# Kernel optimization log

Hardware: AMD Instinct MI355X
Metric: run time of the kernel (lower is better)

Reference implementation:

```python
import jax, jax.numpy as jnp
import numpy as np

HEADS = 16

def setup_inputs() -> dict:
    key = jax.random.key(0)
    ks = jax.random.split(key, 7)
    B, S, E = 2, 2048, 1024
    return {
        "query": jax.random.normal(ks[0], (B, S, E), dtype=jnp.float32),
        "key": jax.random.normal(ks[1], (B, S, E), dtype=jnp.float32),
        "value": jax.random.normal(ks[2], (B, S, E), dtype=jnp.float32),
        "Wqkv": jax.random.normal(ks[3], (E, 3 * E), dtype=jnp.float32) * (E ** -0.5),
        "bqkv": jax.random.normal(ks[4], (3 * E,), dtype=jnp.float32) * 0.02,
        "Wproj": jax.random.normal(ks[5], (E, E), dtype=jnp.float32) * (E ** -0.5),
        "bproj": jax.random.normal(ks[6], (E,), dtype=jnp.float32) * 0.02,
    }

def reference(query, key, value, Wqkv, bqkv, Wproj, bproj):
    # key/value args are unused in the original forward (overwritten by QKV split)
    B, S, E = query.shape
    H = HEADS
    hd = E // H
    qkv = query @ Wqkv + bqkv                     # [B, S, 3E]
    qkv = qkv.reshape(B, S, H, 3 * hd).transpose(0, 2, 1, 3)  # [B, H, S, 3hd]
    q = qkv[..., :hd]
    k = qkv[..., hd:2 * hd]
    v = qkv[..., 2 * hd:]
    qk = jnp.einsum("bhqd,bhkd->bhqk", q, k)
    # faithful quirk: original divides by head_dim**-0.5, i.e. multiplies by sqrt(hd)
    scaled = qk / (hd ** -0.5)
    attn = jax.nn.softmax(scaled, axis=-1)        # dropout p=0 -> identity
    out = jnp.einsum("bhqk,bhkd->bhqd", attn, v)  # [B, H, S, hd]
    out = out.transpose(0, 2, 1, 3).reshape(B, S, E)
    return out @ Wproj + bproj
```

## Files before the change

### kernel.cpp

```cpp
#include <hip/hip_runtime.h>
#include <hip/hip_bf16.h>
#include <stdint.h>

typedef __attribute__((ext_vector_type(8))) _Float16 f16x8;
typedef __attribute__((ext_vector_type(4))) _Float16 f16x4;
typedef __attribute__((ext_vector_type(4))) float f32x4;

static constexpr int BATCH = 2;
static constexpr int SEQ = 2048;
static constexpr int EMB = 1024;
static constexpr int NH = 16;
static constexpr int HD_ = 64;

#define AS1 __attribute__((address_space(1)))
#define AS3 __attribute__((address_space(3)))

__device__ __forceinline__ void gload_lds16(const void* g, void* l) {
  __builtin_amdgcn_global_load_lds((const AS1 uint32_t*)g, (AS3 uint32_t*)l, 16, 0, 0);
}

__device__ __forceinline__ f32x4 mfma16(f16x8 a, f16x8 b, f32x4 c) {
  return __builtin_amdgcn_mfma_f32_16x16x32_f16(a, b, c, 0, 0, 0);
}

__device__ __forceinline__ f16x8 swzread(const _Float16* base, int row, int blk) {
  return *(const f16x8*)((const char*)base + row * 128 +
                         ((blk * 16) ^ ((row & 7) << 4)));
}

__global__ __launch_bounds__(256) void k_prep(const float* __restrict__ q,
                                              _Float16* __restrict__ qo,
                                              const float* __restrict__ wqkv,
                                              _Float16* __restrict__ wqkvo,
                                              const float* __restrict__ wproj,
                                              _Float16* __restrict__ wprojo) {
  __shared__ float tile[32][33];
  const int blk = blockIdx.x;
  const int t = threadIdx.x;
  if (blk < 4096) {
    const int idx = blk * 256 + t;
    float4 v = reinterpret_cast<const float4*>(q)[idx];
    const float* f = reinterpret_cast<const float*>(&v);
    _Float16 h[4];
#pragma unroll
    for (int i = 0; i < 4; ++i) h[i] = (_Float16)f[i];
    reinterpret_cast<uint2*>(qo)[idx] = *reinterpret_cast<uint2*>(h);
    return;
  }
  const float* in;
  _Float16* out;
  int R, C, bx, by;
  bool perm;
  if (blk < 4096 + 3072) {
    const int lo = blk - 4096;
    bx = lo % 96;
    by = lo / 96;
    in = wqkv; out = wqkvo; R = 1024; C = 3072; perm = true;
  } else {
    const int lo = blk - 7168;
    bx = lo & 31;
    by = lo >> 5;
    in = wproj; out = wprojo; R = 1024; C = 1024; perm = false;
  }
  const int tr = t >> 5, tc = t & 31;
  const int r0 = by * 32, c0 = bx * 32;
#pragma unroll
  for (int rr = 0; rr < 32; rr += 8)
    tile[tr + rr][tc] = in[(size_t)(r0 + tr + rr) * C + c0 + tc];
  __syncthreads();
#pragma unroll
  for (int rr = 0; rr < 32; rr += 8) {
    const int c = c0 + tr + rr;
    int d = c;
    if (perm) {
      const int h = c / 192, r = c - h * 192;
      d = (r < 64) ? h * 64 + r
                   : (r < 128 ? 1024 + h * 64 + (r - 64) : 2048 + h * 64 + (r - 128));
    }
    out[(size_t)d * R + r0 + tc] = (_Float16)tile[tc][tr + rr];
  }
}

__global__ __launch_bounds__(512, 1) void k_gemm_qkv(const _Float16* __restrict__ A,
                                                     const _Float16* __restrict__ Bt,
                                                     const float* __restrict__ bias,
                                                     _Float16* __restrict__ oq,
                                                     _Float16* __restrict__ ok,
                                                     _Float16* __restrict__ ov) {
  constexpr int K = EMB;
  __shared__ _Float16 As[2][2][128 * 64];
  __shared__ _Float16 Bs[2][2][128 * 64];
  const int t = threadIdx.x;
  const int l = t & 63, w = t >> 6;
  const int lr = l & 15, lg = l >> 4;
  const int wm = w >> 2, wn = w & 3;
  const int id = blockIdx.x;
  const int xcd = id & 7, wg = id >> 3;
  const int m0 = (xcd * 2 + wg / 12) * 256;
  const int n0 = (wg % 12) * 256;

  const int sr0 = t >> 3, scb = t & 7;
  auto stageA = [&](int buf, int half, int kt) {
    const _Float16* g = A + (size_t)(m0 + half * 128) * K + kt * 64;
    _Float16* d = &As[buf][half][0];
    gload_lds16(g + (size_t)sr0 * K + (scb ^ (sr0 & 7)) * 8, d + sr0 * 64 + scb * 8);
    const int r1 = sr0 + 64;
    gload_lds16(g + (size_t)r1 * K + (scb ^ (r1 & 7)) * 8, d + r1 * 64 + scb * 8);
  };
  auto stageB = [&](int buf, int half, int kt) {
    const _Float16* g = Bt + (size_t)(n0 + half * 128) * K + kt * 64;
    _Float16* d = &Bs[buf][half][0];
    gload_lds16(g + (size_t)sr0 * K + (scb ^ (sr0 & 7)) * 8, d + sr0 * 64 + scb * 8);
    const int r1 = sr0 + 64;
    gload_lds16(g + (size_t)r1 * K + (scb ^ (r1 & 7)) * 8, d + r1 * 64 + scb * 8);
  };

  f32x4 acc[8][4];
#pragma unroll
  for (int m = 0; m < 8; ++m)
#pragma unroll
    for (int n = 0; n < 4; ++n) acc[m][n] = f32x4{0.f, 0.f, 0.f, 0.f};

  stageA(0, 0, 0);
  stageA(0, 1, 0);
  stageB(0, 0, 0);
  stageB(0, 1, 0);

  const int bhh = wn >> 1, brow0 = (wn & 1) * 64;
  f16x8 bf[4][2];

  for (int pair = 0; pair < 8; ++pair) {
#pragma unroll
    for (int ph = 0; ph < 8; ++ph) {
      const int buf = ph >> 2, q = ph & 3;
      bool issued = true;
      if (ph < 4) {
        const int kt = 2 * pair + 1;
        if (q == 0) stageA(1, 0, kt);
        else if (q == 1) stageA(1, 1, kt);
        else if (q == 2) stageB(1, 0, kt);
        else stageB(1, 1, kt);
      } else if (pair + 1 < 8) {
        const int kt = 2 * pair + 2;
        if (q == 0) stageA(0, 0, kt);
        else if (q == 1) stageA(0, 1, kt);
        else if (q == 2) stageB(0, 0, kt);
        else stageB(0, 1, kt);
      } else {
        issued = false;
      }
      if (q == 0) {
        if (issued)
          asm volatile("s_waitcnt vmcnt(2)" ::: "memory");
        else
          asm volatile("s_waitcnt vmcnt(0)" ::: "memory");
        __builtin_amdgcn_s_barrier();
#pragma unroll
        for (int nf = 0; nf < 4; ++nf)
#pragma unroll
          for (int ks = 0; ks < 2; ++ks)
            bf[nf][ks] = swzread(&Bs[buf][bhh][0], brow0 + nf * 16 + lr, ks * 4 + lg);
      }
      f16x8 af[2][2];
#pragma unroll
      for (int dm = 0; dm < 2; ++dm)
#pragma unroll
        for (int ks = 0; ks < 2; ++ks)
          af[dm][ks] = swzread(&As[buf][wm][0], (q * 2 + dm) * 16 + lr, ks * 4 + lg);
      __builtin_amdgcn_s_setprio(1);
#pragma unroll
      for (int dm = 0; dm < 2; ++dm)
#pragma unroll
        for (int nf = 0; nf < 4; ++nf)
#pragma unroll
          for (int ks = 0; ks < 2; ++ks)
            acc[q * 2 + dm][nf] =
                mfma16(af[dm][ks], bf[nf][ks], acc[q * 2 + dm][nf]);
      __builtin_amdgcn_s_setprio(0);
      __builtin_amdgcn_s_barrier();
    }
  }

  const int sec = n0 >> 10;
#pragma unroll
  for (int mf = 0; mf < 8; ++mf) {
#pragma unroll
    for (int nf = 0; nf < 4; ++nf) {
      const int col = n0 + wn * 64 + nf * 16 + lr;
      const int cc = col & 1023;
      const int h = cc >> 6, r = cc & 63;
      const float bv = bias[h * 192 + sec * 64 + r];
      const int row0 = m0 + wm * 128 + mf * 16 + lg * 4;
      const int b = row0 >> 11, s0 = row0 & (SEQ - 1);
      if (sec == 2) {
        f16x4 vv;
#pragma unroll
        for (int i = 0; i < 4; ++i) vv[i] = (_Float16)(acc[mf][nf][i] + bv);
        *(f16x4*)&ov[(((size_t)b * NH + h) * HD_ + r) * SEQ + s0] = vv;
      } else {
#pragma unroll
        for (int i = 0; i < 4; ++i) {
          const float v = acc[mf][nf][i] + bv;
          const size_t dst = (((size_t)b * NH + h) * SEQ + s0 + i) * HD_ + r;
          if (sec == 0)
            oq[dst] = (_Float16)(v * 11.5415603f);
          else
            ok[dst] = (_Float16)v;
        }
      }
    }
  }
}

__global__ __launch_bounds__(256) void k_gemm_proj(const _Float16* __restrict__ A,
                                                   const _Float16* __restrict__ Bt,
                                                   const float* __restrict__ bias,
                                                   float* __restrict__ of) {
  constexpr int K = EMB, N = EMB;
  __shared__ _Float16 As[2][128 * 32];
  __shared__ _Float16 Bs[2][128 * 32];
  const int t = threadIdx.x;
  const int l = t & 63, w = t >> 6;
  const int lr = l & 15, lg = l >> 4;
  const int wr = w >> 1, wc = w & 1;
  const int id = blockIdx.x;
  const int xcd = id & 7, wg = id >> 3;
  const int m0 = (xcd * 4 + wg / 8) * 128;
  const int n0 = (wg & 7) * 128;

  auto stage = [&](int buf, int k0) {
#pragma unroll
    for (int j = 0; j < 2; ++j) {
      const int c = t + 256 * j;
      const int row = c >> 2, cb = c & 3;
      gload_lds16(A + (size_t)(m0 + row) * K + k0 + cb * 8, &As[buf][c * 8]);
      gload_lds16(Bt + (size_t)(n0 + row) * K + k0 + cb * 8, &Bs[buf][c * 8]);
    }
  };

  f32x4 acc[4][4];
#pragma unroll
  for (int m = 0; m < 4; ++m)
#pragma unroll
    for (int n = 0; n < 4; ++n) acc[m][n] = f32x4{0.f, 0.f, 0.f, 0.f};

  stage(0, 0);
  const int NT = K / 32;
  int cur = 0;
  for (int kt = 0; kt < NT; ++kt) {
    __syncthreads();
    if (kt + 1 < NT) stage(cur ^ 1, (kt + 1) * 32);
    f16x8 af[4], bf[4];
#pragma unroll
    for (int m = 0; m < 4; ++m)
      af[m] = *(const f16x8*)&As[cur][(wr * 64 + m * 16 + lr) * 32 + lg * 8];
#pragma unroll
    for (int n = 0; n < 4; ++n)
      bf[n] = *(const f16x8*)&Bs[cur][(wc * 64 + n * 16 + lr) * 32 + lg * 8];
#pragma unroll
    for (int m = 0; m < 4; ++m)
#pragma unroll
      for (int n = 0; n < 4; ++n) acc[m][n] = mfma16(af[m], bf[n], acc[m][n]);
    cur ^= 1;
  }

#pragma unroll
  for (int m = 0; m < 4; ++m)
#pragma unroll
    for (int n = 0; n < 4; ++n)
#pragma unroll
      for (int i = 0; i < 4; ++i) {
        const int row = m0 + wr * 64 + m * 16 + lg * 4 + i;
        const int col = n0 + wc * 64 + n * 16 + lr;
        of[(size_t)row * N + col] = acc[m][n][i] + bias[col];
      }
}

__global__ __launch_bounds__(512) void k_attn(const _Float16* __restrict__ qs,
                                              const _Float16* __restrict__ ks,
                                              const _Float16* __restrict__ vt,
                                              _Float16* __restrict__ ao) {
  __shared__ _Float16 Kt[3][64][64];
  __shared__ _Float16 Vt[3][64][64];
  __shared__ _Float16 Pl[8][16][64];
  const int t = threadIdx.x;
  const int l = t & 63, w = t >> 6;
  const int lr = l & 15, lg = l >> 4;
  const int id = blockIdx.x;
  const int xc = id & 7, m_ = id >> 3;
  const int bh = xc + 8 * (m_ >> 4);
  const int qb = (m_ & 15) * 128 + w * 16;

  const size_t qoff = ((size_t)bh * SEQ + qb + lr) * HD_;
  const f16x8 qf0 = *(const f16x8*)(qs + qoff + lg * 8);
  const f16x8 qf1 = *(const f16x8*)(qs + qoff + 32 + lg * 8);

  const _Float16* kbase = ks + (size_t)bh * SEQ * HD_;
  const _Float16* vbase = vt + (size_t)bh * HD_ * SEQ;

  const int srow = t >> 3, scb = t & 7;
  auto stage = [&](const int buf, const int kv0) {
    gload_lds16(kbase + (size_t)(kv0 + srow) * HD_ + (scb ^ (srow & 7)) * 8,
                &Kt[buf][srow][scb * 8]);
    gload_lds16(vbase + (size_t)srow * SEQ + kv0 + (scb ^ (srow & 7)) * 8,
                &Vt[buf][srow][scb * 8]);
  };

  stage(0, 0);
  stage(1, 64);

  float mr = -1e30f, lsum = 0.f;
  f32x4 oacc[4];
#pragma unroll
  for (int n = 0; n < 4; ++n) oacc[n] = f32x4{0.f, 0.f, 0.f, 0.f};

  const int NT = SEQ / 64;
  int cur = 0;
  for (int it = 0; it < NT; ++it) {
    if (it == NT - 1)
      asm volatile("s_waitcnt vmcnt(0)" ::: "memory");
    else
      asm volatile("s_waitcnt vmcnt(2)" ::: "memory");
    __builtin_amdgcn_s_barrier();
    if (it + 2 < NT) {
      int nb = cur + 2;
      if (nb >= 3) nb -= 3;
      stage(nb, (it + 2) * 64);
    }

    f32x4 sa[4];
    __builtin_amdgcn_s_setprio(1);
#pragma unroll
    for (int t4 = 0; t4 < 4; ++t4) {
      const int r = t4 * 16 + lr;
      const f16x8 kf0 = swzread(&Kt[cur][0][0], r, lg);
      const f16x8 kf1 = swzread(&Kt[cur][0][0], r, lg + 4);
      f32x4 s = mfma16(kf0, qf0, f32x4{0.f, 0.f, 0.f, 0.f});
      sa[t4] = mfma16(kf1, qf1, s);
    }
    __builtin_amdgcn_s_setprio(0);

    float t01 = fmaxf(fmaxf(sa[0][0], sa[0][1]), fmaxf(sa[0][2], sa[0][3]));
    float t23 = fmaxf(fmaxf(sa[1][0], sa[1][1]), fmaxf(sa[1][2], sa[1][3]));
    float t45 = fmaxf(fmaxf(sa[2][0], sa[2][1]), fmaxf(sa[2][2], sa[2][3]));
    float t67 = fmaxf(fmaxf(sa[3][0], sa[3][1]), fmaxf(sa[3][2], sa[3][3]));
    float tm = fmaxf(fmaxf(t01, t23), fmaxf(t45, t67));
    tm = fmaxf(tm, __shfl_xor(tm, 16));
    tm = fmaxf(tm, __shfl_xor(tm, 32));

    if (__all(tm < mr - 24.0f)) {
      cur = (cur + 1 == 3) ? 0 : cur + 1;
      continue;
    }

    if (__any(tm > mr + 8.0f)) {
      const float nm = fmaxf(mr, tm);
      const float corr = exp2f(mr - nm);
      mr = nm;
      lsum *= corr;
      float cb4[4];
#pragma unroll
      for (int i = 0; i < 4; ++i)
        cb4[i] = __shfl(corr, (l & 48) + ((l >> 4) << 2) + i);
#pragma unroll
      for (int n = 0; n < 4; ++n)
#pragma unroll
        for (int i = 0; i < 4; ++i) oacc[n][i] *= cb4[i];
    }

    float ts = 0.f;
    char* plbase = (char*)&Pl[w][0][0];
#pragma unroll
    for (int t4 = 0; t4 < 4; ++t4) {
      f16x4 pp;
#pragma unroll
      for (int i = 0; i < 4; ++i) {
        const float p = exp2f(sa[t4][i] - mr);
        ts += p;
        pp[i] = (_Float16)p;
      }
      *(f16x4*)(plbase + lr * 128 + ((t4 * 32 + lg * 8) ^ ((lr & 7) << 4))) = pp;
    }
    ts += __shfl_xor(ts, 16);
    ts += __shfl_xor(ts, 32);
    lsum += ts;

    const f16x8 aP0 = swzread(&Pl[w][0][0], lr, lg);
    const f16x8 aP1 = swzread(&Pl[w][0][0], lr, lg + 4);
    __builtin_amdgcn_s_setprio(1);
#pragma unroll
    for (int n = 0; n < 4; ++n) {
      const int d = n * 16 + lr;
      const f16x8 bv0 = swzread(&Vt[cur][0][0], d, lg);
      const f16x8 bv1 = swzread(&Vt[cur][0][0], d, lg + 4);
      oacc[n] = mfma16(aP0, bv0, oacc[n]);
      oacc[n] = mfma16(aP1, bv1, oacc[n]);
    }
    __builtin_amdgcn_s_setprio(0);

    cur = (cur + 1 == 3) ? 0 : cur + 1;
  }

  float ls4[4];
#pragma unroll
  for (int i = 0; i < 4; ++i)
    ls4[i] = __shfl(lsum, (l & 48) + ((l >> 4) << 2) + i);
  const int b = bh >> 4, h = bh & 15;
#pragma unroll
  for (int n = 0; n < 4; ++n)
#pragma unroll
    for (int i = 0; i < 4; ++i) {
      const int row = qb + ((l >> 4) << 2) + i;
      ao[((size_t)b * SEQ + row) * EMB + h * HD_ + n * 16 + lr] =
          (_Float16)(oacc[n][i] / ls4[i]);
    }
}

extern "C" void kernel_launch(void* const* d_in, const int* in_sizes, int n_in,
                              void* d_out, int out_size, void* d_ws, size_t ws_size,
                              hipStream_t stream) {
  const float* query = (const float*)d_in[0];
  const float* Wqkv = (const float*)d_in[3];
  const float* bqkv = (const float*)d_in[4];
  const float* Wproj = (const float*)d_in[5];
  const float* bproj = (const float*)d_in[6];
  float* out = (float*)d_out;

  char* ws = (char*)d_ws;
  const size_t MB = 1024 * 1024;
  _Float16* q_f16   = (_Float16*)(ws + 0);
  _Float16* Wqkv_t  = (_Float16*)(ws + 16 * MB);
  _Float16* q_s     = (_Float16*)(ws + 24 * MB);
  _Float16* k_s     = (_Float16*)(ws + 32 * MB);
  _Float16* v_t     = (_Float16*)(ws + 40 * MB);
  _Float16* Wproj_t = (_Float16*)(ws + 48 * MB);
  _Float16* a_o     = (_Float16*)(ws + 51 * MB);

  const int M = BATCH * SEQ;
  k_prep<<<dim3(8192), 256, 0, stream>>>(query, q_f16, Wqkv, Wqkv_t, Wproj, Wproj_t);
  k_gemm_qkv<<<dim3(192), 512, 0, stream>>>(q_f16, Wqkv_t, bqkv, q_s, k_s, v_t);
  k_attn<<<dim3(512), 512, 0, stream>>>(q_s, k_s, v_t, a_o);
  k_gemm_proj<<<dim3(256), 256, 0, stream>>>(a_o, Wproj_t, bproj, out);
}
```

Measured before the change: 145.1 us.

## Switch attention KV staging to double-buffered 128-key tiles with one barrier

```diff
diff --git a/kernel.cpp b/kernel.cpp
--- a/kernel.cpp
+++ b/kernel.cpp
@@ -280,8 +280,8 @@
                                               const _Float16* __restrict__ ks,
                                               const _Float16* __restrict__ vt,
                                               _Float16* __restrict__ ao) {
-  __shared__ _Float16 Kt[3][64][64];
-  __shared__ _Float16 Vt[3][64][64];
+  __shared__ _Float16 Kt[2][128][64];
+  __shared__ _Float16 Vt[2][2][64][64];
   __shared__ _Float16 Pl[8][16][64];
   const int t = threadIdx.x;
   const int l = t & 63, w = t >> 6;
@@ -302,103 +302,97 @@
   auto stage = [&](const int buf, const int kv0) {
     gload_lds16(kbase + (size_t)(kv0 + srow) * HD_ + (scb ^ (srow & 7)) * 8,
                 &Kt[buf][srow][scb * 8]);
+    const int r1 = srow + 64;
+    gload_lds16(kbase + (size_t)(kv0 + r1) * HD_ + (scb ^ (srow & 7)) * 8,
+                &Kt[buf][r1][scb * 8]);
     gload_lds16(vbase + (size_t)srow * SEQ + kv0 + (scb ^ (srow & 7)) * 8,
-                &Vt[buf][srow][scb * 8]);
+                &Vt[buf][0][srow][scb * 8]);
+    gload_lds16(vbase + (size_t)srow * SEQ + kv0 + 64 + (scb ^ (srow & 7)) * 8,
+                &Vt[buf][1][srow][scb * 8]);
   };
 
   stage(0, 0);
-  stage(1, 64);
 
   float mr = -1e30f, lsum = 0.f;
   f32x4 oacc[4];
 #pragma unroll
   for (int n = 0; n < 4; ++n) oacc[n] = f32x4{0.f, 0.f, 0.f, 0.f};
 
-  const int NT = SEQ / 64;
-  int cur = 0;
+  char* plbase = (char*)&Pl[w][0][0];
+  const int NT = SEQ / 128;
   for (int it = 0; it < NT; ++it) {
-    if (it == NT - 1)
-      asm volatile("s_waitcnt vmcnt(0)" ::: "memory");
-    else
-      asm volatile("s_waitcnt vmcnt(2)" ::: "memory");
-    __builtin_amdgcn_s_barrier();
-    if (it + 2 < NT) {
-      int nb = cur + 2;
-      if (nb >= 3) nb -= 3;
-      stage(nb, (it + 2) * 64);
-    }
-
-    f32x4 sa[4];
-    __builtin_amdgcn_s_setprio(1);
-#pragma unroll
-    for (int t4 = 0; t4 < 4; ++t4) {
-      const int r = t4 * 16 + lr;
-      const f16x8 kf0 = swzread(&Kt[cur][0][0], r, lg);
-      const f16x8 kf1 = swzread(&Kt[cur][0][0], r, lg + 4);
-      f32x4 s = mfma16(kf0, qf0, f32x4{0.f, 0.f, 0.f, 0.f});
-      sa[t4] = mfma16(kf1, qf1, s);
-    }
-    __builtin_amdgcn_s_setprio(0);
-
-    float t01 = fmaxf(fmaxf(sa[0][0], sa[0][1]), fmaxf(sa[0][2], sa[0][3]));
-    float t23 = fmaxf(fmaxf(sa[1][0], sa[1][1]), fmaxf(sa[1][2], sa[1][3]));
-    float t45 = fmaxf(fmaxf(sa[2][0], sa[2][1]), fmaxf(sa[2][2], sa[2][3]));
-    float t67 = fmaxf(fmaxf(sa[3][0], sa[3][1]), fmaxf(sa[3][2], sa[3][3]));
-    float tm = fmaxf(fmaxf(t01, t23), fmaxf(t45, t67));
-    tm = fmaxf(tm, __shfl_xor(tm, 16));
-    tm = fmaxf(tm, __shfl_xor(tm, 32));
-
-    if (__all(tm < mr - 24.0f)) {
-      cur = (cur + 1 == 3) ? 0 : cur + 1;
-      continue;
-    }
-
-    if (__any(tm > mr + 8.0f)) {
-      const float nm = fmaxf(mr, tm);
-      const float corr = exp2f(mr - nm);
-      mr = nm;
-      lsum *= corr;
-      float cb4[4];
-#pragma unroll
-      for (int i = 0; i < 4; ++i)
-        cb4[i] = __shfl(corr, (l & 48) + ((l >> 4) << 2) + i);
-#pragma unroll
-      for (int n = 0; n < 4; ++n)
-#pragma unroll
-        for (int i = 0; i < 4; ++i) oacc[n][i] *= cb4[i];
-    }
-
-    float ts = 0.f;
-    char* plbase = (char*)&Pl[w][0][0];
-#pragma unroll
-    for (int t4 = 0; t4 < 4; ++t4) {
-      f16x4 pp;
-#pragma unroll
-      for (int i = 0; i < 4; ++i) {
-        const float p = exp2f(sa[t4][i] - mr);
-        ts += p;
-        pp[i] = (_Float16)p;
-      }
-      *(f16x4*)(plbase + lr * 128 + ((t4 * 32 + lg * 8) ^ ((lr & 7) << 4))) = pp;
-    }
-    ts += __shfl_xor(ts, 16);
-    ts += __shfl_xor(ts, 32);
-    lsum += ts;
-
-    const f16x8 aP0 = swzread(&Pl[w][0][0], lr, lg);
-    const f16x8 aP1 = swzread(&Pl[w][0][0], lr, lg + 4);
-    __builtin_amdgcn_s_setprio(1);
-#pragma unroll
-    for (int n = 0; n < 4; ++n) {
-      const int d = n * 16 + lr;
-      const f16x8 bv0 = swzread(&Vt[cur][0][0], d, lg);
-      const f16x8 bv1 = swzread(&Vt[cur][0][0], d, lg + 4);
-      oacc[n] = mfma16(aP0, bv0, oacc[n]);
-      oacc[n] = mfma16(aP1, bv1, oacc[n]);
-    }
-    __builtin_amdgcn_s_setprio(0);
-
-    cur = (cur + 1 == 3) ? 0 : cur + 1;
+    const int cur = it & 1;
+    __syncthreads();
+    if (it + 1 < NT) stage(cur ^ 1, (it + 1) * 128);
+
+#pragma unroll
+    for (int sub = 0; sub < 2; ++sub) {
+      f32x4 sa[4];
+      __builtin_amdgcn_s_setprio(1);
+#pragma unroll
+      for (int t4 = 0; t4 < 4; ++t4) {
+        const int r = sub * 64 + t4 * 16 + lr;
+        const f16x8 kf0 = swzread(&Kt[cur][0][0], r, lg);
+        const f16x8 kf1 = swzread(&Kt[cur][0][0], r, lg + 4);
+        f32x4 s = mfma16(kf0, qf0, f32x4{0.f, 0.f, 0.f, 0.f});
+        sa[t4] = mfma16(kf1, qf1, s);
+      }
+      __builtin_amdgcn_s_setprio(0);
+
+      float t01 = fmaxf(fmaxf(sa[0][0], sa[0][1]), fmaxf(sa[0][2], sa[0][3]));
+      float t23 = fmaxf(fmaxf(sa[1][0], sa[1][1]), fmaxf(sa[1][2], sa[1][3]));
+      float t45 = fmaxf(fmaxf(sa[2][0], sa[2][1]), fmaxf(sa[2][2], sa[2][3]));
+      float t67 = fmaxf(fmaxf(sa[3][0], sa[3][1]), fmaxf(sa[3][2], sa[3][3]));
+      float tm = fmaxf(fmaxf(t01, t23), fmaxf(t45, t67));
+      tm = fmaxf(tm, __shfl_xor(tm, 16));
+      tm = fmaxf(tm, __shfl_xor(tm, 32));
+
+      if (__all(tm < mr - 24.0f)) continue;
+
+      if (__any(tm > mr + 8.0f)) {
+        const float nm = fmaxf(mr, tm);
+        const float corr = exp2f(mr - nm);
+        mr = nm;
+        lsum *= corr;
+        float cb4[4];
+#pragma unroll
+        for (int i = 0; i < 4; ++i)
+          cb4[i] = __shfl(corr, (l & 48) + ((l >> 4) << 2) + i);
+#pragma unroll
+        for (int n = 0; n < 4; ++n)
+#pragma unroll
+          for (int i = 0; i < 4; ++i) oacc[n][i] *= cb4[i];
+      }
+
+      float ts = 0.f;
+#pragma unroll
+      for (int t4 = 0; t4 < 4; ++t4) {
+        f16x4 pp;
+#pragma unroll
+        for (int i = 0; i < 4; ++i) {
+          const float p = exp2f(sa[t4][i] - mr);
+          ts += p;
+          pp[i] = (_Float16)p;
+        }
+        *(f16x4*)(plbase + lr * 128 + ((t4 * 32 + lg * 8) ^ ((lr & 7) << 4))) = pp;
+      }
+      ts += __shfl_xor(ts, 16);
+      ts += __shfl_xor(ts, 32);
+      lsum += ts;
+
+      const f16x8 aP0 = swzread(&Pl[w][0][0], lr, lg);
+      const f16x8 aP1 = swzread(&Pl[w][0][0], lr, lg + 4);
+      __builtin_amdgcn_s_setprio(1);
+#pragma unroll
+      for (int n = 0; n < 4; ++n) {
+        const int d = n * 16 + lr;
+        const f16x8 bv0 = swzread(&Vt[cur][sub][0][0], d, lg);
+        const f16x8 bv1 = swzread(&Vt[cur][sub][0][0], d, lg + 4);
+        oacc[n] = mfma16(aP0, bv0, oacc[n]);
+        oacc[n] = mfma16(aP1, bv1, oacc[n]);
+      }
+      __builtin_amdgcn_s_setprio(0);
+    }
   }
 
   float ls4[4];
```

After: 143.7 us. Within noise of the previous version (-1.0%).
